# Kernel tuning notes

Measured on AMD Instinct MI355X. Metric: run time of the kernel, lower is better.

The kernel has to match this reference:

```python
import jax, jax.numpy as jnp
import numpy as np
from functools import partial

DIM, HID, DK, NH, SEQ, B = 1024, 512, 512, 4, 16, 2048
DH = DK // NH  # per-head dim = 128
EPS = 1e-5


def _ln(x, g, b):
    m = x.mean(-1, keepdims=True)
    v = ((x - m) ** 2).mean(-1, keepdims=True)
    return (x - m) * jax.lax.rsqrt(v + EPS) * g + b


def setup_inputs() -> dict:
    key = jax.random.key(0)
    ks = jax.random.split(key, 32)
    it = iter(range(32))
    n = lambda shape, s: jax.random.normal(ks[next(it)], shape, jnp.float32) * s
    inp = {
        'visual': n((B, SEQ, DIM), 1.0),
        'text':   n((B, SEQ, DIM), 1.0),
        'user':   n((B, SEQ, DIM), 1.0),
        'cat':    n((B, SEQ, DIM), 1.0),
        'label':  n((B, SEQ, 1), 1.0),
        'h0':     n((B, HID), 1.0),
        'c0':     n((B, HID), 1.0),
        # fusion MLP: Linear(4*dim -> dim)
        'fus_W': n((DIM, 4 * DIM), 1.0 / np.sqrt(4 * DIM)),
        'fus_b': n((DIM,), 0.01),
        # LayerNormLSTM cell params (gate order i,f,g,o)
        'W_ih': n((4 * HID, DIM), 1.0 / np.sqrt(DIM)),
        'W_hh': n((4 * HID, HID), 1.0 / np.sqrt(HID)),
        'g_ih': 1.0 + n((4 * HID,), 0.1), 'b_ih': n((4 * HID,), 0.01),
        'g_hh': 1.0 + n((4 * HID,), 0.1), 'b_hh': n((4 * HID,), 0.01),
        'g_c':  1.0 + n((HID,), 0.1),     'b_c':  n((HID,), 0.01),
        # attention projections
        'wq_W': n((DK, HID), 1.0 / np.sqrt(HID)), 'wq_b': n((DK,), 0.01),
        'wk_W': n((DK, HID), 1.0 / np.sqrt(HID)), 'wk_b': n((DK,), 0.01),
        'wv_W': n((NH, DK, HID), 1.0 / np.sqrt(HID)), 'wv_b': n((NH, DK), 0.01),
        'wout_W': n((DK, DK * NH), 1.0 / np.sqrt(DK * NH)), 'wout_b': n((DK,), 0.01),
        'out_W': n((1, DK), 1.0 / np.sqrt(DK)), 'out_b': n((1,), 0.01),
    }
    return inp


def reference(visual, text, user, cat, label, h0, c0, fus_W, fus_b,
              W_ih, W_hh, g_ih, b_ih, g_hh, b_hh, g_c, b_c,
              wq_W, wq_b, wk_W, wk_b, wv_W, wv_b, wout_W, wout_b, out_W, out_b):
    # fusion MLP (dropout is identity at inference)
    mods = jnp.concatenate([visual, text, user, cat], axis=-1)  # [B,S,4*DIM]
    v_t = jax.nn.relu(mods @ fus_W.T + fus_b)                    # [B,S,DIM]

    # LayerNorm-LSTM recurrence over time via scan
    def step(carry, x_t):
        h, c = carry
        gates = _ln(x_t @ W_ih.T, g_ih, b_ih) + _ln(h @ W_hh.T, g_hh, b_hh)
        i, f, g, o = jnp.split(gates, 4, axis=-1)
        c = jax.nn.sigmoid(f) * c + jax.nn.sigmoid(i) * jnp.tanh(g)
        h = jax.nn.sigmoid(o) * jnp.tanh(_ln(c, g_c, b_c))
        return (h, c), h

    (hn, _), hs = jax.lax.scan(step, (h0, c0), jnp.swapaxes(v_t, 0, 1))
    lstm_out = jnp.swapaxes(hs, 0, 1)  # [B,S,HID]

    # multi-head dot self-attention against final hidden state
    q = (hn @ wq_W.T + wq_b).reshape(-1, NH, DH)                    # [B,H,dh]
    k = (lstm_out @ wk_W.T + wk_b).reshape(-1, SEQ, NH, DH)         # [B,S,H,dh]
    scores = jnp.einsum('bshd,bhd->bhs', k, q) / np.sqrt(DH)        # [B,H,S]
    attn = jax.nn.softmax(scores, axis=-1)
    # per-head full-width values: V[b,h,s,k]
    V = jnp.einsum('hkd,bsd->bhsk', wv_W, lstm_out) + wv_b[None, :, None, :]
    ctx = jnp.einsum('bhsk,bhs->bhk', V, attn).reshape(-1, NH * DK)  # [B,H*DK]
    out_h = ctx @ wout_W.T + wout_b                                  # [B,DK]
    output = out_h @ out_W.T + out_b                                 # [B,1]

    label_one = label[:, -1, 0]
    loss = jnp.mean((output.reshape(-1) - label_one) ** 2)
    return loss, output
```

## Files before the change

kernel.cpp:

```cpp
#include <hip/hip_runtime.h>
#include <cstdint>

#define B_SZ 2048
#define SEQ  16
#define DIM  1024
#define HID  512
#define DK   512
#define NH   4
#define DH   128
#define GATE 2048
#define EPSV 1e-5f

typedef __bf16 bf8_t __attribute__((ext_vector_type(8)));
typedef float  f4_t  __attribute__((ext_vector_type(4)));
typedef unsigned short u16x8 __attribute__((ext_vector_type(8)));
typedef unsigned short u16x4 __attribute__((ext_vector_type(4)));

__device__ __forceinline__ unsigned short f2bf(float f){
  __bf16 h = (__bf16)f;
  return __builtin_bit_cast(unsigned short, h);
}
__device__ __forceinline__ float bf2f(unsigned short u){
  return __builtin_bit_cast(float, ((unsigned int)u) << 16);
}
__device__ __forceinline__ float sigm(float x){ return 1.f/(1.f+__expf(-x)); }
__device__ __forceinline__ float tanh_f(float x){ return 1.f - 2.f/(__expf(2.f*x)+1.f); }

__device__ __forceinline__ void gload16(const void* g, void* l){
  __builtin_amdgcn_global_load_lds(
      (const __attribute__((address_space(1))) void*)g,
      (__attribute__((address_space(3))) void*)l, 16, 0, 0);
}

template<bool OUT_BF16, bool BIAS, bool RELU>
__global__ __launch_bounds__(512, 1) void gemm8p(
    const unsigned short* __restrict__ A,
    const unsigned short* __restrict__ Bw,
    const float* __restrict__ bias,
    void* __restrict__ Cp,
    int N, int K, int nwg)
{
  __shared__ __align__(16) unsigned short As[2][256*64];
  __shared__ __align__(16) unsigned short Bs[2][256*64];
  const int tid = threadIdx.x, lane = tid & 63, w = tid >> 6;
  const int bid = blockIdx.x;
  const int swz = (bid & 7)*(nwg >> 3) + (bid >> 3);
  const int nx  = N >> 8;
  const int lnx = 31 - __clz(nx);
  const int bm0 = (swz >> lnx) << 8;
  const int bn0 = (swz & (nx-1)) << 8;

  const int l8  = lane >> 3;
  const int gsw = (lane & 7) ^ l8;
  const int fr  = lane & 15, kg = lane >> 4;
  const int wm  = (w >> 2)*128, wn = (w & 3)*64;
  const int KT  = K >> 6;

  auto stA = [&](int buf, int kt, int h){
    #pragma unroll
    for (int c=0;c<2;++c){
      const int rb = h*128 + c*64 + w*8;
      gload16(A + (size_t)(bm0 + rb + l8)*K + (size_t)kt*64 + gsw*8, &As[buf][rb*64]);
    }
  };
  auto stB = [&](int buf, int kt, int h){
    #pragma unroll
    for (int c=0;c<2;++c){
      const int rb = h*128 + c*64 + w*8;
      gload16(Bw + (size_t)(bn0 + rb + l8)*K + (size_t)kt*64 + gsw*8, &Bs[buf][rb*64]);
    }
  };
  auto rdA = [&](int buf, int m, int kk)->bf8_t{
    return *(const bf8_t*)&As[buf][(wm + m*16 + fr)*64 + (((kk*4+kg) ^ (fr&7))*8)];
  };
  auto rdB = [&](int buf, int n, int kk)->bf8_t{
    return *(const bf8_t*)&Bs[buf][(wn + n*16 + fr)*64 + (((kk*4+kg) ^ (fr&7))*8)];
  };

  f4_t acc[8][4];
  #pragma unroll
  for (int m=0;m<8;++m)
    #pragma unroll
    for (int n=0;n<4;++n) acc[m][n] = (f4_t)0.f;

  bf8_t bfr[4][2];

  auto mfma2 = [&](int m0, const bf8_t a00, const bf8_t a01,
                   const bf8_t a10, const bf8_t a11){
    __builtin_amdgcn_s_setprio(1);
    #pragma unroll
    for (int n=0;n<4;++n){
      acc[m0][n]   = __builtin_amdgcn_mfma_f32_16x16x32_bf16(a00, bfr[n][0], acc[m0][n],   0,0,0);
      acc[m0][n]   = __builtin_amdgcn_mfma_f32_16x16x32_bf16(a01, bfr[n][1], acc[m0][n],   0,0,0);
      acc[m0+1][n] = __builtin_amdgcn_mfma_f32_16x16x32_bf16(a10, bfr[n][0], acc[m0+1][n], 0,0,0);
      acc[m0+1][n] = __builtin_amdgcn_mfma_f32_16x16x32_bf16(a11, bfr[n][1], acc[m0+1][n], 0,0,0);
    }
    __builtin_amdgcn_s_setprio(0);
  };

  auto phase12 = [&](int buf, auto&& stg){
    #pragma unroll
    for (int n=0;n<4;++n){ bfr[n][0]=rdB(buf,n,0); bfr[n][1]=rdB(buf,n,1); }
    const bf8_t a00=rdA(buf,0,0), a01=rdA(buf,0,1), a10=rdA(buf,1,0), a11=rdA(buf,1,1);
    stg();
    asm volatile("s_barrier" ::: "memory");
    mfma2(0, a00,a01,a10,a11);
    asm volatile("s_barrier" ::: "memory");
  };
  auto phase4 = [&](int buf, int m0, auto&& stg, bool vm){
    const bf8_t a00=rdA(buf,m0,0), a01=rdA(buf,m0,1), a10=rdA(buf,m0+1,0), a11=rdA(buf,m0+1,1);
    stg();
    if (vm){
      __builtin_amdgcn_sched_barrier(0);
      asm volatile("s_waitcnt vmcnt(4)" ::: "memory");
    }
    asm volatile("s_barrier" ::: "memory");
    mfma2(m0, a00,a01,a10,a11);
    asm volatile("s_barrier" ::: "memory");
  };

  stA(0,0,0); stA(0,0,1); stB(0,0,0); stB(0,0,1);
  stB(1,1,0); stB(1,1,1);
  __builtin_amdgcn_sched_barrier(0);
  asm volatile("s_waitcnt vmcnt(4)" ::: "memory");
  asm volatile("s_barrier" ::: "memory");

  const int NIT = KT >> 1;
  for (int it=0; it<NIT; ++it){
    const int t0 = 2*it, t1 = t0+1;
    const int tN  = (t0+2 < KT) ? t0+2 : KT-1;
    const int tB3 = (t1+2 < KT) ? t1+2 : KT-1;

    phase12(0,      [&]{ stA(1,t1,0);  });
    phase4 (0, 2,   [&]{ stA(1,t1,1);  }, false);
    phase4 (0, 4,   [&]{ stB(0,tN,0);  }, false);
    phase4 (0, 6,   [&]{ stB(0,tN,1);  }, true);
    phase12(1,      [&]{ stA(0,tN,0);  });
    phase4 (1, 2,   [&]{ stA(0,tN,1);  }, false);
    phase4 (1, 4,   [&]{ stB(1,tB3,0); }, false);
    phase4 (1, 6,   [&]{ stB(1,tB3,1); }, true);
  }

  #pragma unroll
  for (int n=0;n<4;++n){
    const int col = bn0 + wn + n*16 + fr;
    float bv = 0.f;
    if constexpr (BIAS) bv = bias[col];
    #pragma unroll
    for (int m=0;m<8;++m){
      #pragma unroll
      for (int j=0;j<4;++j){
        const int row = bm0 + wm + m*16 + kg*4 + j;
        float v = acc[m][n][j] + bv;
        if constexpr (RELU) v = fmaxf(v, 0.f);
        if constexpr (OUT_BF16) ((unsigned short*)Cp)[(size_t)row*N + col] = f2bf(v);
        else                    ((float*)Cp)[(size_t)row*N + col] = v;
      }
    }
  }
}

__global__ __launch_bounds__(512, 1) void gemm8pf(
    const float* __restrict__ A0, const float* __restrict__ A1,
    const float* __restrict__ A2, const float* __restrict__ A3,
    const unsigned short* __restrict__ Bw,
    const float* __restrict__ bias,
    unsigned short* __restrict__ Cp,
    int N, int K, int nwg)
{
  __shared__ __align__(16) unsigned short As[2][256*64];
  __shared__ __align__(16) unsigned short Bs[2][256*64];
  const int tid = threadIdx.x, lane = tid & 63, w = tid >> 6;
  const int bid = blockIdx.x;
  const int swz = (bid & 7)*(nwg >> 3) + (bid >> 3);
  const int nx  = N >> 8;
  const int lnx = 31 - __clz(nx);
  const int bm0 = (swz >> lnx) << 8;
  const int bn0 = (swz & (nx-1)) << 8;

  const int l8  = lane >> 3;
  const int gsw = (lane & 7) ^ l8;
  const int fr  = lane & 15, kg = lane >> 4;
  const int wm  = (w >> 2)*128, wn = (w & 3)*64;
  const int KT  = K >> 6;

  auto stB = [&](int buf, int kt, int h){
    #pragma unroll
    for (int c=0;c<2;++c){
      const int rb = h*128 + c*64 + w*8;
      gload16(Bw + (size_t)(bn0 + rb + l8)*K + (size_t)kt*64 + gsw*8, &Bs[buf][rb*64]);
    }
  };

  f4_t rg[4];
  auto ldA = [&](int kt, int h){
    const int kb = kt*64, si = kb >> 10, kc = kb & 1023;
    const float* Asel = si==0?A0 : si==1?A1 : si==2?A2 : A3;
    const float* p = Asel + (size_t)(bm0 + h*128 + (tid>>2))*1024 + kc + (tid&3)*16;
    rg[0] = *(const f4_t*)p;     rg[1] = *(const f4_t*)(p+4);
    rg[2] = *(const f4_t*)(p+8); rg[3] = *(const f4_t*)(p+12);
  };
  auto wrA = [&](int buf, int h){
    const int row = h*128 + (tid>>2);
    const int s = row & 7, g0 = (tid&3)*2;
    u16x8 w0, w1;
    #pragma unroll
    for (int j=0;j<4;++j){
      w0[j]=f2bf(rg[0][j]); w0[4+j]=f2bf(rg[1][j]);
      w1[j]=f2bf(rg[2][j]); w1[4+j]=f2bf(rg[3][j]);
    }
    *(u16x8*)&As[buf][row*64 + ((g0^s)*8)]     = w0;
    *(u16x8*)&As[buf][row*64 + (((g0+1)^s)*8)] = w1;
  };

  auto rdA = [&](int buf, int m, int kk)->bf8_t{
    return *(const bf8_t*)&As[buf][(wm + m*16 + fr)*64 + (((kk*4+kg) ^ (fr&7))*8)];
  };
  auto rdB = [&](int buf, int n, int kk)->bf8_t{
    return *(const bf8_t*)&Bs[buf][(wn + n*16 + fr)*64 + (((kk*4+kg) ^ (fr&7))*8)];
  };

  f4_t acc[8][4];
  #pragma unroll
  for (int m=0;m<8;++m)
    #pragma unroll
    for (int n=0;n<4;++n) acc[m][n] = (f4_t)0.f;

  bf8_t bfr[4][2];

  auto mfma2 = [&](int m0, const bf8_t a00, const bf8_t a01,
                   const bf8_t a10, const bf8_t a11){
    __builtin_amdgcn_s_setprio(1);
    #pragma unroll
    for (int n=0;n<4;++n){
      acc[m0][n]   = __builtin_amdgcn_mfma_f32_16x16x32_bf16(a00, bfr[n][0], acc[m0][n],   0,0,0);
      acc[m0][n]   = __builtin_amdgcn_mfma_f32_16x16x32_bf16(a01, bfr[n][1], acc[m0][n],   0,0,0);
      acc[m0+1][n] = __builtin_amdgcn_mfma_f32_16x16x32_bf16(a10, bfr[n][0], acc[m0+1][n], 0,0,0);
      acc[m0+1][n] = __builtin_amdgcn_mfma_f32_16x16x32_bf16(a11, bfr[n][1], acc[m0+1][n], 0,0,0);
    }
    __builtin_amdgcn_s_setprio(0);
  };

  auto phase12 = [&](int buf, auto&& stg){
    #pragma unroll
    for (int n=0;n<4;++n){ bfr[n][0]=rdB(buf,n,0); bfr[n][1]=rdB(buf,n,1); }
    const bf8_t a00=rdA(buf,0,0), a01=rdA(buf,0,1), a10=rdA(buf,1,0), a11=rdA(buf,1,1);
    stg();
    asm volatile("s_barrier" ::: "memory");
    mfma2(0, a00,a01,a10,a11);
    asm volatile("s_barrier" ::: "memory");
  };
  auto phase4 = [&](int buf, int m0, auto&& stg, bool vm){
    const bf8_t a00=rdA(buf,m0,0), a01=rdA(buf,m0,1), a10=rdA(buf,m0+1,0), a11=rdA(buf,m0+1,1);
    stg();
    if (vm){
      __builtin_amdgcn_sched_barrier(0);
      asm volatile("s_waitcnt vmcnt(4)" ::: "memory");
    }
    asm volatile("s_barrier" ::: "memory");
    mfma2(m0, a00,a01,a10,a11);
    asm volatile("s_barrier" ::: "memory");
  };

  stB(0,0,0); stB(0,0,1); stB(1,1,0); stB(1,1,1);
  ldA(0,0); wrA(0,0); ldA(0,1); wrA(0,1);
  asm volatile("s_waitcnt lgkmcnt(0)" ::: "memory");
  asm volatile("s_waitcnt vmcnt(0)" ::: "memory");
  asm volatile("s_barrier" ::: "memory");

  const int NIT = KT >> 1;
  for (int it=0; it<NIT; ++it){
    const int t0 = 2*it, t1 = t0+1;
    const int tN  = (t0+2 < KT) ? t0+2 : KT-1;
    const int tB3 = (t1+2 < KT) ? t1+2 : KT-1;

    phase12(0,      [&]{ ldA(t1,0); });
    phase4 (0, 2,   [&]{ wrA(1,0); ldA(t1,1); }, false);
    phase4 (0, 4,   [&]{ wrA(1,1); stB(0,tN,0); }, false);
    phase4 (0, 6,   [&]{ stB(0,tN,1);
                         asm volatile("s_waitcnt lgkmcnt(0)":::"memory"); }, true);
    phase12(1,      [&]{ ldA(tN,0); });
    phase4 (1, 2,   [&]{ wrA(0,0); ldA(tN,1); }, false);
    phase4 (1, 4,   [&]{ wrA(0,1); stB(1,tB3,0); }, false);
    phase4 (1, 6,   [&]{ stB(1,tB3,1);
                         asm volatile("s_waitcnt lgkmcnt(0)":::"memory"); }, true);
  }

  #pragma unroll
  for (int n=0;n<4;++n){
    const int col = bn0 + wn + n*16 + fr;
    const float bv = bias[col];
    #pragma unroll
    for (int m=0;m<8;++m){
      #pragma unroll
      for (int j=0;j<4;++j){
        const int row = bm0 + wm + m*16 + kg*4 + j;
        float v = fmaxf(acc[m][n][j] + bv, 0.f);
        Cp[(size_t)row*N + col] = f2bf(v);
      }
    }
  }
}

template<bool OUT_BF16, bool BIAS>
__global__ __launch_bounds__(256) void gemm64(
    const unsigned short* __restrict__ A,
    const unsigned short* __restrict__ Bw,
    const float* __restrict__ bias,
    void* __restrict__ Cp,
    int N, int K, int nwg)
{
  __shared__ __align__(16) unsigned short As[64*64];
  __shared__ __align__(16) unsigned short Bs[64*64];
  const int tid = threadIdx.x, lane = tid & 63, wave = tid >> 6;
  const int bid = blockIdx.x;
  const int swz = (bid & 7)*(nwg >> 3) + (bid >> 3);
  const int nx  = N >> 6;
  const int lnx = 31 - __clz(nx);
  const int bm0 = (swz >> lnx) << 6;
  const int bn0 = (swz & (nx-1)) << 6;

  const int r8  = lane >> 3;
  const int gsw = ((lane & 7) ^ r8) * 8;
  const unsigned short* Ab = A  + (size_t)(bm0 + wave*16 + r8)*K + gsw;
  const unsigned short* Bb = Bw + (size_t)(bn0 + wave*16 + r8)*K + gsw;
  unsigned short* la = As + wave*1024;
  unsigned short* lb = Bs + wave*1024;

  f4_t acc[2][2];
  #pragma unroll
  for (int m=0;m<2;++m)
    #pragma unroll
    for (int n=0;n<2;++n) acc[m][n] = (f4_t)0.f;

  const int KT = K >> 6;
  const int fr = lane & 15, kg = lane >> 4;
  const int wm = (wave & 1)*32, wn = (wave >> 1)*32;

  for (int kt = 0; kt < KT; ++kt){
    if (kt) __syncthreads();
    const size_t ko = (size_t)kt*64;
    #pragma unroll
    for (int q = 0; q < 2; ++q){
      gload16(Ab + ko + (size_t)q*8*K, la + q*512);
      gload16(Bb + ko + (size_t)q*8*K, lb + q*512);
    }
    __syncthreads();
    #pragma unroll
    for (int kk = 0; kk < 2; ++kk){
      bf8_t af[2], bf_[2];
      #pragma unroll
      for (int m=0;m<2;++m){
        const int r = wm+m*16+fr;
        af[m]  = *(const bf8_t*)&As[r*64 + (((kk*4+kg) ^ (r&7))*8)];
      }
      #pragma unroll
      for (int n=0;n<2;++n){
        const int r = wn+n*16+fr;
        bf_[n] = *(const bf8_t*)&Bs[r*64 + (((kk*4+kg) ^ (r&7))*8)];
      }
      #pragma unroll
      for (int m=0;m<2;++m)
        #pragma unroll
        for (int n=0;n<2;++n)
          acc[m][n] = __builtin_amdgcn_mfma_f32_16x16x32_bf16(af[m], bf_[n], acc[m][n], 0,0,0);
    }
  }

  #pragma unroll
  for (int n=0;n<2;++n){
    const int col = bn0 + wn + n*16 + fr;
    float bv = 0.f;
    if constexpr (BIAS) bv = bias[col];
    #pragma unroll
    for (int m=0;m<2;++m){
      #pragma unroll
      for (int j=0;j<4;++j){
        const int row = bm0 + wm + m*16 + kg*4 + j;
        float v = acc[m][n][j] + bv;
        if constexpr (OUT_BF16) ((unsigned short*)Cp)[(size_t)row*N + col] = f2bf(v);
        else                    ((float*)Cp)[(size_t)row*N + col] = v;
      }
    }
  }
}

__global__ __launch_bounds__(256) void lstm_step(
  const unsigned short* __restrict__ X, const unsigned short* __restrict__ Gh,
  const float* __restrict__ c_src, float* __restrict__ c_dst,
  const float* __restrict__ g_ih, const float* __restrict__ b_ih,
  const float* __restrict__ g_hh, const float* __restrict__ b_hh,
  const float* __restrict__ g_c,  const float* __restrict__ b_c,
  unsigned short* __restrict__ h_out, unsigned short* __restrict__ lstm_out,
  int t)
{
  const int b = blockIdx.x, tid = threadIdx.x;
  __shared__ float xs[GATE];
  __shared__ float gs[GATE];
  __shared__ float red[32];
  const unsigned short* xrow = X  + ((size_t)b*SEQ + t)*GATE;
  const unsigned short* grow = Gh + (size_t)b*GATE;
  u16x8 xv = *(const u16x8*)&xrow[tid*8];
  u16x8 gv = *(const u16x8*)&grow[tid*8];
  float sx=0,sx2=0,sg=0,sg2=0;
  #pragma unroll
  for (int j=0;j<8;++j){
    float x = bf2f(xv[j]), g = bf2f(gv[j]);
    xs[tid*8+j]=x; gs[tid*8+j]=g;
    sx += x; sx2 += x*x; sg += g; sg2 += g*g;
  }
  #pragma unroll
  for (int m=32;m;m>>=1){
    sx += __shfl_xor(sx,m); sx2 += __shfl_xor(sx2,m);
    sg += __shfl_xor(sg,m); sg2 += __shfl_xor(sg2,m);
  }
  const int w = tid>>6;
  if ((tid&63)==0){ red[w]=sx; red[4+w]=sx2; red[8+w]=sg; red[12+w]=sg2; }
  __syncthreads();
  sx  = red[0]+red[1]+red[2]+red[3];
  sx2 = red[4]+red[5]+red[6]+red[7];
  sg  = red[8]+red[9]+red[10]+red[11];
  sg2 = red[12]+red[13]+red[14]+red[15];
  const float mX = sx*(1.f/GATE), mH = sg*(1.f/GATE);
  const float rX = rsqrtf(sx2*(1.f/GATE)-mX*mX+EPSV);
  const float rH = rsqrtf(sg2*(1.f/GATE)-mH*mH+EPSV);

  float cN[2], xo[2]; float sc=0, sc2=0;
  #pragma unroll
  for (int rep=0;rep<2;++rep){
    const int n = tid + rep*256;
    const int ni=n, nf=n+HID, ng=n+2*HID, no=n+3*HID;
    float gi = (xs[ni]-mX)*rX*g_ih[ni]+b_ih[ni] + (gs[ni]-mH)*rH*g_hh[ni]+b_hh[ni];
    float gf = (xs[nf]-mX)*rX*g_ih[nf]+b_ih[nf] + (gs[nf]-mH)*rH*g_hh[nf]+b_hh[nf];
    float gg = (xs[ng]-mX)*rX*g_ih[ng]+b_ih[ng] + (gs[ng]-mH)*rH*g_hh[ng]+b_hh[ng];
    float go = (xs[no]-mX)*rX*g_ih[no]+b_ih[no] + (gs[no]-mH)*rH*g_hh[no]+b_hh[no];
    float co = c_src[(size_t)b*HID + n];
    float cn = sigm(gf)*co + sigm(gi)*tanh_f(gg);
    cN[rep]=cn; xo[rep]=go;
    sc += cn; sc2 += cn*cn;
  }
  #pragma unroll
  for (int m=32;m;m>>=1){ sc += __shfl_xor(sc,m); sc2 += __shfl_xor(sc2,m); }
  if ((tid&63)==0){ red[16+w]=sc; red[20+w]=sc2; }
  __syncthreads();
  sc  = red[16]+red[17]+red[18]+red[19];
  sc2 = red[20]+red[21]+red[22]+red[23];
  const float mC = sc*(1.f/HID);
  const float rC = rsqrtf(sc2*(1.f/HID)-mC*mC+EPSV);
  #pragma unroll
  for (int rep=0;rep<2;++rep){
    const int n = tid + rep*256;
    float hN = sigm(xo[rep])*tanh_f((cN[rep]-mC)*rC*g_c[n]+b_c[n]);
    c_dst[(size_t)b*HID+n] = cN[rep];
    unsigned short hbv = f2bf(hN);
    h_out[(size_t)b*HID+n] = hbv;
    lstm_out[((size_t)b*SEQ+t)*HID+n] = hbv;
  }
}

__global__ __launch_bounds__(256) void attn_out_k(
  const float* __restrict__ q, const unsigned short* __restrict__ Km,
  const unsigned short* __restrict__ lo_all,
  const float* __restrict__ u, const float* __restrict__ Cc,
  float* __restrict__ out)
{
  const int b = blockIdx.x, tid = threadIdx.x;
  __shared__ float qs[DK];
  __shared__ float sc[NH][SEQ];
  __shared__ float at[NH][SEQ];
  __shared__ float red[4];
  for (int i=tid; i<DK; i+=256) qs[i] = q[(size_t)b*DK + i];
  __syncthreads();
  {
    const int p = tid>>2, sub = tid&3, h = p>>4, s = p&15;
    const unsigned short* krow = Km + ((size_t)b*SEQ + s)*DK + h*DH + sub*32;
    const float* qh = &qs[h*DH + sub*32];
    float part = 0.f;
    #pragma unroll
    for (int c8=0;c8<4;++c8){
      u16x8 kv = *(const u16x8*)(krow + c8*8);
      #pragma unroll
      for (int j=0;j<8;++j) part += qh[c8*8+j]*bf2f(kv[j]);
    }
    part += __shfl_xor(part,1); part += __shfl_xor(part,2);
    if (sub==0) sc[h][s] = part * 0.08838834764831845f;
  }
  __syncthreads();
  if (tid < 64){
    const int h = tid>>4;
    float v = sc[h][tid&15], mx = v;
    #pragma unroll
    for (int m=1;m<16;m<<=1) mx = fmaxf(mx, __shfl_xor(mx,m));
    float e = __expf(v-mx), se = e;
    #pragma unroll
    for (int m=1;m<16;m<<=1) se += __shfl_xor(se,m);
    at[h][tid&15] = e/se;
  }
  __syncthreads();
  float accum = 0.f;
  #pragma unroll
  for (int it=0; it<4; ++it){
    const int idx = it*256 + tid;
    const int h = idx>>8, d0 = (idx&255)*2;
    const unsigned short* lo = lo_all + (size_t)b*SEQ*HID + d0;
    float p0=0.f, p1=0.f;
    #pragma unroll
    for (int s=0;s<16;++s){
      unsigned int pr = *(const unsigned int*)(lo + s*HID);
      float a = at[h][s];
      p0 += a*bf2f((unsigned short)(pr&0xffffu));
      p1 += a*bf2f((unsigned short)(pr>>16));
    }
    accum += u[h*HID+d0]*p0 + u[h*HID+d0+1]*p1;
  }
  #pragma unroll
  for (int m=32;m;m>>=1) accum += __shfl_xor(accum,m);
  if ((tid&63)==0) red[tid>>6] = accum;
  __syncthreads();
  if (tid==0) out[1+b] = red[0]+red[1]+red[2]+red[3] + Cc[0];
}

__global__ __launch_bounds__(256) void loss_k(const float* __restrict__ label, float* __restrict__ out){
  const int tid = threadIdx.x;
  __shared__ float red[4];
  float s = 0.f;
  for (int b=tid; b<B_SZ; b+=256){
    float d = out[1+b] - label[(size_t)b*SEQ + (SEQ-1)];
    s += d*d;
  }
  #pragma unroll
  for (int m=32;m;m>>=1) s += __shfl_xor(s,m);
  if ((tid&63)==0) red[tid>>6]=s;
  __syncthreads();
  if (tid==0) out[0] = (red[0]+red[1]+red[2]+red[3]) * (1.f/B_SZ);
}

__global__ __launch_bounds__(256) void cvt_bf16_k(const float* __restrict__ in, unsigned short* __restrict__ o, int n){
  int i = (blockIdx.x*256 + threadIdx.x)*4;
  if (i < n){
    f4_t v = *(const f4_t*)&in[i];
    u16x4 w;
    #pragma unroll
    for (int j=0;j<4;++j) w[j] = f2bf(v[j]);
    *(u16x4*)&o[i] = w;
  }
}

__global__ __launch_bounds__(256) void fold_we_k(
  const float* __restrict__ wout_W, const float* __restrict__ out_W, float* __restrict__ we)
{
  const int j = blockIdx.x*256 + threadIdx.x;
  float s=0.f;
  for (int m=0;m<512;++m) s += out_W[m]*wout_W[(size_t)m*2048+j];
  we[j]=s;
}
__global__ __launch_bounds__(256) void fold_u_k(
  const float* __restrict__ we, const float* __restrict__ wv_W, float* __restrict__ u)
{
  const int o = blockIdx.x*256 + threadIdx.x;
  const int h = o>>9, d = o&511;
  const float* wv = wv_W + (size_t)h*262144 + d;
  const float* wp = we + h*512;
  float s=0.f;
  for (int k=0;k<512;++k) s += wp[k]*wv[(size_t)k*512];
  u[o]=s;
}
__global__ __launch_bounds__(256) void fold_c_k(
  const float* __restrict__ we, const float* __restrict__ wv_b,
  const float* __restrict__ out_W, const float* __restrict__ wout_b,
  const float* __restrict__ out_b, float* __restrict__ Cc)
{
  const int tid = threadIdx.x;
  __shared__ float red[4];
  float s=0.f;
  for (int j=tid;j<2048;j+=256) s += we[j]*wv_b[j];
  for (int m=tid;m<512;m+=256)  s += out_W[m]*wout_b[m];
  #pragma unroll
  for (int m=32;m;m>>=1) s += __shfl_xor(s,m);
  if ((tid&63)==0) red[tid>>6]=s;
  __syncthreads();
  if (tid==0) Cc[0] = red[0]+red[1]+red[2]+red[3] + out_b[0];
}

extern "C" void kernel_launch(void* const* d_in, const int* in_sizes, int n_in,
                              void* d_out, int out_size, void* d_ws, size_t ws_size,
                              hipStream_t stream)
{
  const float* visual = (const float*)d_in[0];
  const float* text   = (const float*)d_in[1];
  const float* user_  = (const float*)d_in[2];
  const float* cat_   = (const float*)d_in[3];
  const float* label  = (const float*)d_in[4];
  const float* h0     = (const float*)d_in[5];
  const float* c0     = (const float*)d_in[6];
  const float* fus_W  = (const float*)d_in[7];
  const float* fus_b  = (const float*)d_in[8];
  const float* W_ih   = (const float*)d_in[9];
  const float* W_hh   = (const float*)d_in[10];
  const float* g_ih   = (const float*)d_in[11];
  const float* b_ih   = (const float*)d_in[12];
  const float* g_hh   = (const float*)d_in[13];
  const float* b_hh   = (const float*)d_in[14];
  const float* g_c    = (const float*)d_in[15];
  const float* b_c    = (const float*)d_in[16];
  const float* wq_W   = (const float*)d_in[17];
  const float* wq_b   = (const float*)d_in[18];
  const float* wk_W   = (const float*)d_in[19];
  const float* wk_b   = (const float*)d_in[20];
  const float* wv_W   = (const float*)d_in[21];
  const float* wv_b   = (const float*)d_in[22];
  const float* wout_W = (const float*)d_in[23];
  const float* wout_b = (const float*)d_in[24];
  const float* out_W  = (const float*)d_in[25];
  const float* out_b  = (const float*)d_in[26];
  (void)in_sizes; (void)n_in; (void)out_size; (void)ws_size;

  char* base = (char*)d_ws; size_t off = 0;
  auto alloc = [&](size_t n)->void*{ void* p = base+off; off += n; off = (off+255)&~(size_t)255; return p; };
  unsigned short* X     = (unsigned short*)alloc((size_t)32768*2048*2);
  unsigned short* vt    = (unsigned short*)alloc((size_t)32768*1024*2);
  unsigned short* lo    = (unsigned short*)alloc((size_t)32768*512*2);
  unsigned short* Km    = (unsigned short*)alloc((size_t)32768*512*2);
  unsigned short* Gh    = (unsigned short*)alloc((size_t)2048*2048*2);
  float*          cws   = (float*)         alloc((size_t)2048*512*4);
  unsigned short* hb    = (unsigned short*)alloc((size_t)2048*512*2);
  float*          qb    = (float*)         alloc((size_t)2048*512*4);
  unsigned short* fusWb = (unsigned short*)alloc((size_t)1024*4096*2);
  unsigned short* Wihb  = (unsigned short*)alloc((size_t)2048*1024*2);
  unsigned short* Whhb  = (unsigned short*)alloc((size_t)2048*512*2);
  unsigned short* wqb   = (unsigned short*)alloc((size_t)512*512*2);
  unsigned short* wkb   = (unsigned short*)alloc((size_t)512*512*2);
  float*          we_ws = (float*)         alloc(2048*4);
  float*          u_ws  = (float*)         alloc(2048*4);
  float*          C_ws  = (float*)         alloc(256);

  cvt_bf16_k<<<dim3(4096), dim3(256), 0, stream>>>(fus_W, fusWb, 1024*4096);
  cvt_bf16_k<<<dim3(2048), dim3(256), 0, stream>>>(W_ih,  Wihb,  2048*1024);
  cvt_bf16_k<<<dim3(1024), dim3(256), 0, stream>>>(W_hh,  Whhb,  2048*512);
  cvt_bf16_k<<<dim3(256),  dim3(256), 0, stream>>>(wq_W,  wqb,   512*512);
  cvt_bf16_k<<<dim3(256),  dim3(256), 0, stream>>>(wk_W,  wkb,   512*512);
  cvt_bf16_k<<<dim3(1024), dim3(256), 0, stream>>>(h0,    hb,    2048*512);
  fold_we_k<<<dim3(8), dim3(256), 0, stream>>>(wout_W, out_W, we_ws);
  fold_u_k <<<dim3(8), dim3(256), 0, stream>>>(we_ws, wv_W, u_ws);
  fold_c_k <<<dim3(1), dim3(256), 0, stream>>>(we_ws, wv_b, out_W, wout_b, out_b, C_ws);

  gemm8pf<<<dim3(512), dim3(512), 0, stream>>>(
      visual, text, user_, cat_, fusWb, fus_b, vt, 1024, 4096, 512);
  gemm8p<true,false,false><<<dim3(1024), dim3(512), 0, stream>>>(
      vt, Wihb, nullptr, X, 2048, 1024, 1024);

  for (int t=0; t<SEQ; ++t){
    gemm64<true,false><<<dim3(1024), dim3(256), 0, stream>>>(
        hb, Whhb, nullptr, Gh, 2048, 512, 1024);
    lstm_step<<<dim3(2048), dim3(256), 0, stream>>>(
        X, Gh, (t==0 ? c0 : cws), cws, g_ih, b_ih, g_hh, b_hh, g_c, b_c, hb, lo, t);
  }

  gemm64<false,true><<<dim3(256), dim3(256), 0, stream>>>(
      hb, wqb, wq_b, qb, 512, 512, 256);
  gemm8p<true,true,false><<<dim3(256), dim3(512), 0, stream>>>(
      lo, wkb, wk_b, Km, 512, 512, 256);

  attn_out_k<<<dim3(2048), dim3(256), 0, stream>>>(qb, Km, lo, u_ws, C_ws, (float*)d_out);
  loss_k<<<dim3(1), dim3(256), 0, stream>>>(label, (float*)d_out);
}
```

Measured before the change: 978.3 us.

## Split fp32 A-tile staging into quarter loads spread across MMA phases

The fusion GEMM's A operand (fp32 activations converted to bf16) is now loaded in four 64-row quarters using two register sets. Each quarter's global load and LDS write is interleaved across the eight MFMA phases. The explicit vmcnt waits are removed and the prologue preloads the next tile's first quarters. This spreads global-load latency more evenly and lowers register pressure per stage. It relies on implicit waits for correctness, which adds some risk in the ordering of vmcnt.

Result: faster. 945.5 us (-3.4%).

```diff
diff --git a/kernel.cpp b/kernel.cpp
--- a/kernel.cpp
+++ b/kernel.cpp
@@ -192,25 +192,20 @@
     }
   };
 
-  f4_t rg[4];
-  auto ldA = [&](int kt, int h){
+  f4_t rgA[2], rgB[2];
+  auto ldQ = [&](f4_t* rg, int kt, int q){
     const int kb = kt*64, si = kb >> 10, kc = kb & 1023;
     const float* Asel = si==0?A0 : si==1?A1 : si==2?A2 : A3;
-    const float* p = Asel + (size_t)(bm0 + h*128 + (tid>>2))*1024 + kc + (tid&3)*16;
-    rg[0] = *(const f4_t*)p;     rg[1] = *(const f4_t*)(p+4);
-    rg[2] = *(const f4_t*)(p+8); rg[3] = *(const f4_t*)(p+12);
-  };
-  auto wrA = [&](int buf, int h){
-    const int row = h*128 + (tid>>2);
-    const int s = row & 7, g0 = (tid&3)*2;
-    u16x8 w0, w1;
-    #pragma unroll
-    for (int j=0;j<4;++j){
-      w0[j]=f2bf(rg[0][j]); w0[4+j]=f2bf(rg[1][j]);
-      w1[j]=f2bf(rg[2][j]); w1[4+j]=f2bf(rg[3][j]);
-    }
-    *(u16x8*)&As[buf][row*64 + ((g0^s)*8)]     = w0;
-    *(u16x8*)&As[buf][row*64 + (((g0+1)^s)*8)] = w1;
+    const float* p = Asel + (size_t)(bm0 + q*64 + (tid>>3))*1024 + kc + (tid&7)*8;
+    rg[0] = *(const f4_t*)p; rg[1] = *(const f4_t*)(p+4);
+  };
+  auto wrQ = [&](const f4_t* rg, int buf, int q){
+    const int R = q*64 + (tid>>3);
+    const int g = (tid&7) ^ (R&7);
+    u16x8 wv;
+    #pragma unroll
+    for (int j=0;j<4;++j){ wv[j]=f2bf(rg[0][j]); wv[4+j]=f2bf(rg[1][j]); }
+    *(u16x8*)&As[buf][R*64 + g*8] = wv;
   };
 
   auto rdA = [&](int buf, int m, int kk)->bf8_t{
@@ -250,40 +245,44 @@
     mfma2(0, a00,a01,a10,a11);
     asm volatile("s_barrier" ::: "memory");
   };
-  auto phase4 = [&](int buf, int m0, auto&& stg, bool vm){
+  auto phase4 = [&](int buf, int m0, auto&& stg){
     const bf8_t a00=rdA(buf,m0,0), a01=rdA(buf,m0,1), a10=rdA(buf,m0+1,0), a11=rdA(buf,m0+1,1);
     stg();
-    if (vm){
-      __builtin_amdgcn_sched_barrier(0);
-      asm volatile("s_waitcnt vmcnt(4)" ::: "memory");
-    }
     asm volatile("s_barrier" ::: "memory");
     mfma2(m0, a00,a01,a10,a11);
     asm volatile("s_barrier" ::: "memory");
   };
 
   stB(0,0,0); stB(0,0,1); stB(1,1,0); stB(1,1,1);
-  ldA(0,0); wrA(0,0); ldA(0,1); wrA(0,1);
+  ldQ(rgA,0,0); ldQ(rgB,0,1); wrQ(rgA,0,0); wrQ(rgB,0,1);
+  ldQ(rgA,0,2); ldQ(rgB,0,3); wrQ(rgA,0,2); wrQ(rgB,0,3);
+  ldQ(rgA,1,0); ldQ(rgB,1,1);
   asm volatile("s_waitcnt lgkmcnt(0)" ::: "memory");
-  asm volatile("s_waitcnt vmcnt(0)" ::: "memory");
+  asm volatile("s_waitcnt vmcnt(2)" ::: "memory");
   asm volatile("s_barrier" ::: "memory");
 
   const int NIT = KT >> 1;
   for (int it=0; it<NIT; ++it){
-    const int t0 = 2*it, t1 = t0+1;
-    const int tN  = (t0+2 < KT) ? t0+2 : KT-1;
+    const int t1  = 2*it+1;
+    const int tN  = (t1+1 < KT) ? t1+1 : KT-1;
     const int tB3 = (t1+2 < KT) ? t1+2 : KT-1;
 
-    phase12(0,      [&]{ ldA(t1,0); });
-    phase4 (0, 2,   [&]{ wrA(1,0); ldA(t1,1); }, false);
-    phase4 (0, 4,   [&]{ wrA(1,1); stB(0,tN,0); }, false);
-    phase4 (0, 6,   [&]{ stB(0,tN,1);
-                         asm volatile("s_waitcnt lgkmcnt(0)":::"memory"); }, true);
-    phase12(1,      [&]{ ldA(tN,0); });
-    phase4 (1, 2,   [&]{ wrA(0,0); ldA(tN,1); }, false);
-    phase4 (1, 4,   [&]{ wrA(0,1); stB(1,tB3,0); }, false);
-    phase4 (1, 6,   [&]{ stB(1,tB3,1);
-                         asm volatile("s_waitcnt lgkmcnt(0)":::"memory"); }, true);
+    phase12(0, [&]{ wrQ(rgA,1,0); ldQ(rgA,t1,2); });
+    phase4 (0, 2, [&]{ wrQ(rgB,1,1); ldQ(rgB,t1,3); });
+    phase4 (0, 4, [&]{ wrQ(rgA,1,2); ldQ(rgA,tN,0);
+                       __builtin_amdgcn_sched_barrier(0); stB(0,tN,0); });
+    phase4 (0, 6, [&]{ wrQ(rgB,1,3); ldQ(rgB,tN,1);
+                       __builtin_amdgcn_sched_barrier(0); stB(0,tN,1);
+                       __builtin_amdgcn_sched_barrier(0);
+                       asm volatile("s_waitcnt lgkmcnt(0)":::"memory"); });
+    phase12(1, [&]{ wrQ(rgA,0,0); ldQ(rgA,tN,2); });
+    phase4 (1, 2, [&]{ wrQ(rgB,0,1); ldQ(rgB,tN,3); });
+    phase4 (1, 4, [&]{ wrQ(rgA,0,2); ldQ(rgA,tB3,0);
+                       __builtin_amdgcn_sched_barrier(0); stB(1,tB3,0); });
+    phase4 (1, 6, [&]{ wrQ(rgB,0,3); ldQ(rgB,tB3,1);
+                       __builtin_amdgcn_sched_barrier(0); stB(1,tB3,1);
+                       __builtin_amdgcn_sched_barrier(0);
+                       asm volatile("s_waitcnt lgkmcnt(0)":::"memory"); });
   }
 
   #pragma unroll
```
